# Performance work log

Hardware: AMD Instinct MI355X
Metric: run time of the kernel (lower is better)

Reference implementation:

```python
import jax, jax.numpy as jnp
import numpy as np

N, E = 25000, 400000
D, H, L = 64, 4, 3
DH = D  # per-head out dim (concat=False averages heads)
NODE_IN, EDGE_IN = 16, 4


def setup_inputs() -> dict:
    key = jax.random.key(0)
    ks = jax.random.split(key, 24)
    s = 0.05
    inp = {
        "node_feat_in": jax.random.normal(ks[0], (N, NODE_IN), jnp.float32),
        "edge_index_in": jax.random.randint(ks[1], (2, E), 0, N, jnp.int32),
        "edge_attr_in": jax.random.normal(ks[2], (E, EDGE_IN), jnp.float32),
        # initial embeddings
        "W_node": jax.random.normal(ks[3], (NODE_IN, D), jnp.float32) * s,
        "b_node": jnp.zeros((D,), jnp.float32),
        "W_edge": jax.random.normal(ks[4], (EDGE_IN, D), jnp.float32) * s,
        "b_edge": jnp.zeros((D,), jnp.float32),
        # GATv2Conv params, stacked over layers
        "Wl": jax.random.normal(ks[5], (L, D, H * DH), jnp.float32) * s,
        "bl": jnp.zeros((L, H * DH), jnp.float32),
        "Wr": jax.random.normal(ks[6], (L, D, H * DH), jnp.float32) * s,
        "br": jnp.zeros((L, H * DH), jnp.float32),
        "We": jax.random.normal(ks[7], (L, D, H * DH), jnp.float32) * s,
        "att": jax.random.normal(ks[8], (L, H, DH), jnp.float32) * s,
        "conv_b": jnp.zeros((L, D), jnp.float32),
        # LayerNorm
        "ln_g": jnp.ones((L, D), jnp.float32),
        "ln_b": jnp.zeros((L, D), jnp.float32),
        # edge update MLP: Linear(3D->D), ReLU, Linear(D->D)
        "euW1": jax.random.normal(ks[9], (L, 3 * D, D), jnp.float32) * s,
        "eub1": jnp.zeros((L, D), jnp.float32),
        "euW2": jax.random.normal(ks[10], (L, D, D), jnp.float32) * s,
        "eub2": jnp.zeros((L, D), jnp.float32),
    }
    return inp


def _layernorm(x, g, b, eps=1e-5):
    mu = x.mean(-1, keepdims=True)
    var = ((x - mu) ** 2).mean(-1, keepdims=True)
    return (x - mu) * jax.lax.rsqrt(var + eps) * g + b


def _gatv2_conv(x, e, row, col, Wl, bl, Wr, br, We, att, cb):
    # PyG GATv2Conv(concat=False, edge_dim=D), eval mode (no dropout),
    # add_self_loops=True with fill_value='mean' on edge_attr.
    n = x.shape[0]
    xl = (x @ Wl + bl).reshape(n, H, DH)  # source transform
    xr = (x @ Wr + br).reshape(n, H, DH)  # target transform
    # self-loop edge attr = per-target mean of incoming edge attrs
    cnt = jax.ops.segment_sum(jnp.ones((e.shape[0],), x.dtype), col, num_segments=n)
    e_loop = jax.ops.segment_sum(e, col, num_segments=n) / jnp.maximum(cnt, 1.0)[:, None]
    ee = (jnp.concatenate([e, e_loop], 0) @ We).reshape(-1, H, DH)
    loop = jnp.arange(n, dtype=row.dtype)
    rowf = jnp.concatenate([row, loop])
    colf = jnp.concatenate([col, loop])
    msg = xl[rowf] + xr[colf] + ee                      # [E+N, H, DH]
    score = jnp.sum(jax.nn.leaky_relu(msg, 0.2) * att, -1)  # [E+N, H]
    # segment softmax over incoming edges of each target node
    m = jax.ops.segment_max(score, colf, num_segments=n)
    a = jnp.exp(score - m[colf])
    a = a / jax.ops.segment_sum(a, colf, num_segments=n)[colf]
    out = jax.ops.segment_sum(a[..., None] * xl[rowf], colf, num_segments=n)  # [N,H,DH]
    return out.mean(1) + cb  # concat=False -> head mean, plus bias


def reference(node_feat_in, edge_index_in, edge_attr_in, W_node, b_node, W_edge,
              b_edge, Wl, bl, Wr, br, We, att, conv_b, ln_g, ln_b, euW1, eub1,
              euW2, eub2):
    row, col = edge_index_in[0], edge_index_in[1]
    x = jax.nn.relu(node_feat_in @ W_node + b_node)
    e = jax.nn.relu(edge_attr_in @ W_edge + b_edge)
    for i in range(L):
        upd = _gatv2_conv(x, e, row, col, Wl[i], bl[i], Wr[i], br[i], We[i],
                          att[i], conv_b[i])
        x = jax.nn.relu(_layernorm(x + upd, ln_g[i], ln_b[i]))
        eu_in = jnp.concatenate([x[row], x[col], e], -1)  # [E, 3D]
        e_upd = jax.nn.relu(eu_in @ euW1[i] + eub1[i]) @ euW2[i] + eub2[i]
        e = jax.nn.relu(e + e_upd)
    return x, e
```

## Files before the change

### kernel.cpp

```cpp
#include <hip/hip_runtime.h>
#include <hip/hip_bf16.h>
#include <cstdint>
#include <cstddef>

constexpr int kN  = 25000;
constexpr int kE  = 400000;
constexpr int kEN = kE + kN;
constexpr int kD  = 64;
constexpr int kH  = 4;
constexpr int kHD = 256;

typedef __attribute__((ext_vector_type(8))) short short8;
typedef __attribute__((ext_vector_type(4))) float f32x4;

__device__ __forceinline__ float lrelu02(float x){ return x > 0.f ? x : 0.2f*x; }
__device__ __forceinline__ unsigned short f2bf(float f){
  __hip_bfloat16 h = __float2bfloat16(f);
  return *reinterpret_cast<unsigned short*>(&h);
}
__device__ __forceinline__ float bf2f(unsigned short u){
  return __uint_as_float(((unsigned)u) << 16);
}
__device__ __forceinline__ float bf_lo(unsigned u){ return __uint_as_float(u << 16); }
__device__ __forceinline__ float bf_hi(unsigned u){ return __uint_as_float(u & 0xffff0000u); }
__device__ __forceinline__ unsigned pack_bf2(float a, float b){
  return ((unsigned)f2bf(a)) | (((unsigned)f2bf(b)) << 16);
}

__global__ void k_deg(const int* __restrict__ col, int* __restrict__ deg){
  int i = blockIdx.x*256 + threadIdx.x;
  if (i < kE) atomicAdd(&deg[col[i]], 1);
}

__global__ void k_scan(const int* __restrict__ deg, int* __restrict__ col_start){
  __shared__ int lds[1024];
  __shared__ int carry_s;
  int t = threadIdx.x;
  if (t == 0) carry_s = 0;
  __syncthreads();
  for (int base = 0; base < kN; base += 1024){
    int v = (base + t < kN) ? deg[base + t] : 0;
    lds[t] = v; __syncthreads();
    for (int off = 1; off < 1024; off <<= 1){
      int add = (t >= off) ? lds[t - off] : 0;
      __syncthreads();
      lds[t] += add;
      __syncthreads();
    }
    int incl = lds[t];
    int carry = carry_s;
    if (base + t < kN) col_start[base + t] = carry + incl - v;
    __syncthreads();
    if (t == 0) carry_s = carry + lds[1023];
    __syncthreads();
  }
  if (t == 0) col_start[kN] = carry_s;
}

__global__ void k_fill(const int* __restrict__ col, const int* __restrict__ col_start,
                       int* __restrict__ fill, int* __restrict__ edge_ids){
  int i = blockIdx.x*256 + threadIdx.x;
  if (i < kE){
    int c = col[i];
    int p = atomicAdd(&fill[c], 1);
    edge_ids[col_start[c] + p] = i;
  }
}

__global__ void k_permrc(const int* __restrict__ edge_ids, const int* __restrict__ row,
                         const int* __restrict__ col, int* __restrict__ rowp,
                         int2* __restrict__ rc2){
  int p = blockIdx.x*256 + threadIdx.x;
  if (p < kE){
    int eid = edge_ids[p];
    int r = row[eid], c = col[eid];
    rowp[p] = r;
    rc2[p] = make_int2(r, c);
  }
}

__global__ void k_prep(const float* __restrict__ We, unsigned short* __restrict__ WeT){
  int idx = blockIdx.x*256 + threadIdx.x;
  if (idx >= 3*256*64) return;
  int l = idx >> 14, j = (idx >> 6) & 255, k = idx & 63;
  WeT[idx] = f2bf(We[(size_t)l*16384 + k*256 + j]);
}

__global__ void k_prep2(const float* __restrict__ euW1, const float* __restrict__ euW2,
                        unsigned short* __restrict__ W1cT, unsigned short* __restrict__ W2T){
  int idx = blockIdx.x*256 + threadIdx.x;
  if (idx >= 3*64*64) return;
  int l = idx >> 12, rem = idx & 4095, d = rem >> 6, k = rem & 63;
  W1cT[idx] = f2bf(euW1[(size_t)l*192*64 + (size_t)(128+k)*64 + d]);
  W2T[idx]  = f2bf(euW2[(size_t)l*64*64  + (size_t)k*64 + d]);
}

__global__ void k_x0(const float* __restrict__ nf, const float* __restrict__ W,
                     const float* __restrict__ b, float* __restrict__ x){
  int i = blockIdx.x*256 + threadIdx.x;
  if (i >= kN*kD) return;
  int n = i >> 6, d = i & 63;
  float acc = b[d];
#pragma unroll
  for (int k = 0; k < 16; k++) acc += nf[n*16 + k] * W[k*64 + d];
  x[i] = fmaxf(acc, 0.f);
}

__global__ void k_e0p(const int* __restrict__ edge_ids,
                      const float* __restrict__ ea, const float* __restrict__ W,
                      const float* __restrict__ b,
                      unsigned short* __restrict__ ebf_perm){
  long long i = (long long)blockIdx.x*256 + threadIdx.x;
  if (i >= (long long)kE*kD) return;
  int p = (int)(i >> 6), d = (int)(i & 63);
  int eid = edge_ids[p];
  float acc = b[d];
#pragma unroll
  for (int k = 0; k < 4; k++) acc += ea[eid*4 + k] * W[k*64 + d];
  ebf_perm[i] = f2bf(fmaxf(acc, 0.f));
}

#define XLR_NPB 8
__global__ __launch_bounds__(256) void k_xlr(const float* __restrict__ x,
    const float* __restrict__ Wl, const float* __restrict__ bl,
    const float* __restrict__ Wr, const float* __restrict__ br,
    unsigned short* __restrict__ xl_bf, unsigned short* __restrict__ xr_bf){
  __shared__ float xs[XLR_NPB*64];
  int j = threadIdx.x;
  int n0 = blockIdx.x * XLR_NPB;
  for (int i = j; i < XLR_NPB*64; i += 256){
    int n = n0 + (i >> 6);
    xs[i] = (n < kN) ? x[(size_t)n*64 + (i & 63)] : 0.f;
  }
  __syncthreads();
  float accl[XLR_NPB], accr[XLR_NPB];
  float blv = bl[j], brv = br[j];
#pragma unroll
  for (int t = 0; t < XLR_NPB; t++){ accl[t] = blv; accr[t] = brv; }
  for (int k = 0; k < 64; k++){
    float wl = Wl[k*kHD + j], wr = Wr[k*kHD + j];
#pragma unroll
    for (int t = 0; t < XLR_NPB; t++){
      float xv = xs[t*64 + k];
      accl[t] += xv * wl; accr[t] += xv * wr;
    }
  }
#pragma unroll
  for (int t = 0; t < XLR_NPB; t++){
    int n = n0 + t;
    if (n < kN){
      xl_bf[(size_t)n*kHD + j] = f2bf(accl[t]);
      xr_bf[(size_t)n*kHD + j] = f2bf(accr[t]);
    }
  }
}

__global__ __launch_bounds__(256) void k_eloop(const unsigned short* __restrict__ ebf_perm,
    const int* __restrict__ col_start, unsigned short* __restrict__ eloop_bf){
  int wave = threadIdx.x >> 6, lane = threadIdx.x & 63;
  int n = blockIdx.x*4 + wave;
  if (n >= kN) return;
  int s0 = col_start[n], s1 = col_start[n+1];
  float acc = 0.f;
  for (int p = s0; p < s1; p++)
    acc += bf2f(ebf_perm[(size_t)p*64 + lane]);
  int dg = s1 - s0;
  eloop_bf[(size_t)n*64 + lane] = f2bf(acc / (float)(dg > 0 ? dg : 1));
}

#define SC_G 2048
#define SC_MAXT 13
__global__ __launch_bounds__(256) void k_score_mfma(
    const unsigned short* __restrict__ ebf_perm,
    const unsigned short* __restrict__ eloop_bf,
    const unsigned short* __restrict__ xl_bf,
    const unsigned short* __restrict__ xr_bf,
    const int2* __restrict__ rc2,
    const unsigned short* __restrict__ WeT,
    const float* __restrict__ att,
    float* __restrict__ score)
{
  int lane = threadIdx.x & 63;
  int h    = threadIdx.x >> 6;
  int e16  = lane & 15;
  int kb   = lane >> 4;

  short8 A[4][2];
  uint2 attp[4];
#pragma unroll
  for (int mt = 0; mt < 4; mt++){
    const unsigned short* arow = WeT + (size_t)(h*64 + mt*16 + e16)*64 + kb*8;
    A[mt][0] = *(const short8*)(arow);
    A[mt][1] = *(const short8*)(arow + 32);
    f32x4 av = *(const f32x4*)(att + h*64 + mt*16 + kb*4);
    attp[mt].x = pack_bf2(av[0], av[1]);
    attp[mt].y = pack_bf2(av[2], av[3]);
  }

  constexpr int NT = (kEN + 15)/16;
  int t0 = blockIdx.x;

  int2 rcs[SC_MAXT];
#pragma unroll
  for (int t = 0; t < SC_MAXT; t++){
    int tile = t0 + t*SC_G;
    if (tile < NT){
      int p = tile*16 + e16;
      int pc = (p < kEN) ? p : 0;
      if (pc < kE) rcs[t] = rc2[pc];
      else         rcs[t] = make_int2(pc - kE, pc - kE);
    } else {
      rcs[t] = make_int2(0, 0);
    }
  }

#pragma unroll
  for (int t = 0; t < SC_MAXT; t++){
    int tile = t0 + t*SC_G;
    if (tile >= NT) break;
    int p = tile*16 + e16;
    int pc = (p < kEN) ? p : 0;
    bool isE = pc < kE;
    const unsigned short* erow = isE ? (ebf_perm + (size_t)pc*64)
                                     : (eloop_bf + (size_t)(pc - kE)*64);
    short8 b0 = *(const short8*)(erow + kb*8);
    short8 b1 = *(const short8*)(erow + 32 + kb*8);
    const unsigned short* xl_ = xl_bf + (size_t)rcs[t].x*kHD + h*64;
    const unsigned short* xr_ = xr_bf + (size_t)rcs[t].y*kHD + h*64;
    uint2 xlu[4], xru[4];
#pragma unroll
    for (int mt = 0; mt < 4; mt++){
      xlu[mt] = *(const uint2*)(xl_ + mt*16 + kb*4);
      xru[mt] = *(const uint2*)(xr_ + mt*16 + kb*4);
    }
    float sc = 0.f;
#pragma unroll
    for (int mt = 0; mt < 4; mt++){
      f32x4 acc = {0.f,0.f,0.f,0.f};
      acc = __builtin_amdgcn_mfma_f32_16x16x32_bf16(A[mt][0], b0, acc, 0, 0, 0);
      acc = __builtin_amdgcn_mfma_f32_16x16x32_bf16(A[mt][1], b1, acc, 0, 0, 0);
      sc += lrelu02(acc[0] + bf_lo(xlu[mt].x) + bf_lo(xru[mt].x)) * bf_lo(attp[mt].x);
      sc += lrelu02(acc[1] + bf_hi(xlu[mt].x) + bf_hi(xru[mt].x)) * bf_hi(attp[mt].x);
      sc += lrelu02(acc[2] + bf_lo(xlu[mt].y) + bf_lo(xru[mt].y)) * bf_lo(attp[mt].y);
      sc += lrelu02(acc[3] + bf_hi(xlu[mt].y) + bf_hi(xru[mt].y)) * bf_hi(attp[mt].y);
    }
    sc += __shfl_xor(sc, 16);
    sc += __shfl_xor(sc, 32);
    int wp = tile*16 + lane;
    if (lane < 16 && wp < kEN) score[(size_t)wp*kH + h] = sc;
  }
}

__global__ __launch_bounds__(256) void k_agg_ln(
    const unsigned short* __restrict__ xl_bf, const float* __restrict__ score,
    const int* __restrict__ rowp, const int* __restrict__ col_start,
    const float* __restrict__ conv_b, const float* __restrict__ ln_g,
    const float* __restrict__ ln_b, float* __restrict__ x){
  int wv = threadIdx.x >> 6, l = threadIdx.x & 63;
  int n = blockIdx.x*4 + wv;
  if (n >= kN) return;
  int h = l >> 4;
  int s0 = col_start[n], s1 = col_start[n+1];

  float sc_self = score[(size_t)(kE + n)*kH + h];
  float m = sc_self;
  for (int p = s0; p < s1; p++)
    m = fmaxf(m, score[(size_t)p*kH + h]);

  float w0 = __expf(sc_self - m);
  float s = w0;
  float a0, a1, a2, a3;
  {
    uint2 u = *(const uint2*)(xl_bf + (size_t)n*kHD + l*4);
    a0 = w0*bf_lo(u.x); a1 = w0*bf_hi(u.x);
    a2 = w0*bf_lo(u.y); a3 = w0*bf_hi(u.y);
  }
  int p = s0;
  for (; p + 4 <= s1; p += 4){
    float e0 = __expf(score[(size_t)(p+0)*kH + h] - m);
    float e1 = __expf(score[(size_t)(p+1)*kH + h] - m);
    float e2 = __expf(score[(size_t)(p+2)*kH + h] - m);
    float e3 = __expf(score[(size_t)(p+3)*kH + h] - m);
    int r0 = rowp[p], r1 = rowp[p+1], r2 = rowp[p+2], r3 = rowp[p+3];
    uint2 u0 = *(const uint2*)(xl_bf + (size_t)r0*kHD + l*4);
    uint2 u1 = *(const uint2*)(xl_bf + (size_t)r1*kHD + l*4);
    uint2 u2 = *(const uint2*)(xl_bf + (size_t)r2*kHD + l*4);
    uint2 u3 = *(const uint2*)(xl_bf + (size_t)r3*kHD + l*4);
    s += e0 + e1 + e2 + e3;
    a0 += e0*bf_lo(u0.x) + e1*bf_lo(u1.x) + e2*bf_lo(u2.x) + e3*bf_lo(u3.x);
    a1 += e0*bf_hi(u0.x) + e1*bf_hi(u1.x) + e2*bf_hi(u2.x) + e3*bf_hi(u3.x);
    a2 += e0*bf_lo(u0.y) + e1*bf_lo(u1.y) + e2*bf_lo(u2.y) + e3*bf_lo(u3.y);
    a3 += e0*bf_hi(u0.y) + e1*bf_hi(u1.y) + e2*bf_hi(u2.y) + e3*bf_hi(u3.y);
  }
  for (; p < s1; p++){
    float ew = __expf(score[(size_t)p*kH + h] - m);
    int r = rowp[p];
    uint2 u = *(const uint2*)(xl_bf + (size_t)r*kHD + l*4);
    s += ew;
    a0 += ew*bf_lo(u.x); a1 += ew*bf_hi(u.x);
    a2 += ew*bf_lo(u.y); a3 += ew*bf_hi(u.y);
  }
  float inv = 1.f / s;
  a0 *= inv; a1 *= inv; a2 *= inv; a3 *= inv;
  a0 += __shfl_xor(a0, 16); a0 += __shfl_xor(a0, 32);
  a1 += __shfl_xor(a1, 16); a1 += __shfl_xor(a1, 32);
  a2 += __shfl_xor(a2, 16); a2 += __shfl_xor(a2, 32);
  a3 += __shfl_xor(a3, 16); a3 += __shfl_xor(a3, 32);
  int d0 = (l & 15)*4;
  f32x4 cb = *(const f32x4*)(conv_b + d0);
  f32x4 xv = *(const f32x4*)(x + (size_t)n*64 + d0);
  float y0 = xv[0] + a0*0.25f + cb[0];
  float y1 = xv[1] + a1*0.25f + cb[1];
  float y2 = xv[2] + a2*0.25f + cb[2];
  float y3 = xv[3] + a3*0.25f + cb[3];
  float part = y0 + y1 + y2 + y3;
  part += __shfl_xor(part, 1); part += __shfl_xor(part, 2);
  part += __shfl_xor(part, 4); part += __shfl_xor(part, 8);
  float mu = part * (1.f/64.f);
  float f0 = y0 - mu, f1 = y1 - mu, f2 = y2 - mu, f3 = y3 - mu;
  float vp = f0*f0 + f1*f1 + f2*f2 + f3*f3;
  vp += __shfl_xor(vp, 1); vp += __shfl_xor(vp, 2);
  vp += __shfl_xor(vp, 4); vp += __shfl_xor(vp, 8);
  float rstd = rsqrtf(vp * (1.f/64.f) + 1e-5f);
  f32x4 gv = *(const f32x4*)(ln_g + d0);
  f32x4 bv = *(const f32x4*)(ln_b + d0);
  if (l < 16){
    f32x4 o;
    o[0] = fmaxf(f0*rstd*gv[0] + bv[0], 0.f);
    o[1] = fmaxf(f1*rstd*gv[1] + bv[1], 0.f);
    o[2] = fmaxf(f2*rstd*gv[2] + bv[2], 0.f);
    o[3] = fmaxf(f3*rstd*gv[3] + bv[3], 0.f);
    *(f32x4*)(x + (size_t)n*64 + d0) = o;
  }
}

#define PQ_NPB 16
__global__ __launch_bounds__(256) void k_pq(const float* __restrict__ x,
    const float* __restrict__ W1, const float* __restrict__ b1,
    unsigned short* __restrict__ P_bf, unsigned short* __restrict__ Q_bf){
  __shared__ float xs[PQ_NPB*64];
  int tid = threadIdx.x;
  int j = tid & 63;
  int s = tid >> 6;
  int n0 = blockIdx.x * PQ_NPB;
  for (int i = tid; i < PQ_NPB*64; i += 256){
    int n = n0 + (i >> 6);
    xs[i] = (n < kN) ? x[(size_t)n*64 + (i & 63)] : 0.f;
  }
  __syncthreads();
  float accP[4], accQ[4];
  float b1v = b1[j];
#pragma unroll
  for (int t = 0; t < 4; t++){ accP[t] = b1v; accQ[t] = 0.f; }
  for (int k = 0; k < 64; k++){
    float wa = W1[k*64 + j];
    float wb = W1[(64 + k)*64 + j];
#pragma unroll
    for (int t = 0; t < 4; t++){
      float xv = xs[(s*4 + t)*64 + k];
      accP[t] += xv * wa; accQ[t] += xv * wb;
    }
  }
#pragma unroll
  for (int t = 0; t < 4; t++){
    int n = n0 + s*4 + t;
    if (n < kN){
      P_bf[(size_t)n*64 + j] = f2bf(accP[t]);
      Q_bf[(size_t)n*64 + j] = f2bf(accQ[t]);
    }
  }
}

__global__ __launch_bounds__(256) void k_mlp_mfma(
    unsigned short* __restrict__ ebf_perm,
    float* __restrict__ eout_scatter,
    const int* __restrict__ edge_ids,
    const unsigned short* __restrict__ P_bf, const unsigned short* __restrict__ Q_bf,
    const unsigned short* __restrict__ W1cT,
    const unsigned short* __restrict__ W2T,
    const float* __restrict__ b2,
    const int2* __restrict__ rc2)
{
  __shared__ unsigned short Hl[4][1024];
  int lane = threadIdx.x & 63, wv = threadIdx.x >> 6;
  int e16 = lane & 15, g = lane >> 4;
  int swz = (e16 & 7) << 4;
  char* Hw = (char*)Hl[wv];
  bool last = (eout_scatter != nullptr);

  short8 a1[4][2], a2[4][2];
#pragma unroll
  for (int mt = 0; mt < 4; mt++){
#pragma unroll
    for (int c = 0; c < 2; c++){
      a1[mt][c] = *(const short8*)(W1cT + (size_t)(mt*16 + e16)*64 + c*32 + g*8);
      a2[mt][c] = *(const short8*)(W2T  + (size_t)(mt*16 + e16)*64 + c*32 + g*8);
    }
  }
  f32x4 b2v[4];
#pragma unroll
  for (int mt = 0; mt < 4; mt++) b2v[mt] = *(const f32x4*)(b2 + mt*16 + g*4);

  int wid = (blockIdx.x*256 + threadIdx.x) >> 6;
  int nw  = (gridDim.x*256) >> 6;
  for (int tile = wid; tile < kE/16; tile += nw){
    int p = tile*16 + e16;
    int2 rc = rc2[p];
    const unsigned short* erow = ebf_perm + (size_t)p*64;
    short8 eb0 = *(const short8*)(erow + g*8);
    short8 eb1 = *(const short8*)(erow + 32 + g*8);
    const unsigned short* Pr = P_bf + (size_t)rc.x*64;
    const unsigned short* Qc = Q_bf + (size_t)rc.y*64;

#pragma unroll
    for (int mt = 0; mt < 4; mt++){
      f32x4 acc = {0.f,0.f,0.f,0.f};
      acc = __builtin_amdgcn_mfma_f32_16x16x32_bf16(a1[mt][0], eb0, acc, 0, 0, 0);
      acc = __builtin_amdgcn_mfma_f32_16x16x32_bf16(a1[mt][1], eb1, acc, 0, 0, 0);
      uint2 pu = *(const uint2*)(Pr + mt*16 + g*4);
      uint2 qu = *(const uint2*)(Qc + mt*16 + g*4);
      float h0 = fmaxf(acc[0] + bf_lo(pu.x) + bf_lo(qu.x), 0.f);
      float h1 = fmaxf(acc[1] + bf_hi(pu.x) + bf_hi(qu.x), 0.f);
      float h2 = fmaxf(acc[2] + bf_lo(pu.y) + bf_lo(qu.y), 0.f);
      float h3 = fmaxf(acc[3] + bf_hi(pu.y) + bf_hi(qu.y), 0.f);
      uint2 pk; pk.x = pack_bf2(h0, h1); pk.y = pack_bf2(h2, h3);
      *(uint2*)(Hw + (((e16 << 7) + (mt << 5) + (g << 3)) ^ swz)) = pk;
    }
    short8 hb0 = *(const short8*)(Hw + (((e16 << 7)      + (g << 4)) ^ swz));
    short8 hb1 = *(const short8*)(Hw + (((e16 << 7) + 64 + (g << 4)) ^ swz));

    int oe = last ? edge_ids[p] : 0;
#pragma unroll
    for (int mt = 0; mt < 4; mt++){
      f32x4 o = {0.f,0.f,0.f,0.f};
      o = __builtin_amdgcn_mfma_f32_16x16x32_bf16(a2[mt][0], hb0, o, 0, 0, 0);
      o = __builtin_amdgcn_mfma_f32_16x16x32_bf16(a2[mt][1], hb1, o, 0, 0, 0);
      size_t off = (size_t)p*64 + mt*16 + g*4;
      uint2 u = *(const uint2*)(ebf_perm + off);
      f32x4 eo;
      eo[0] = bf_lo(u.x); eo[1] = bf_hi(u.x); eo[2] = bf_lo(u.y); eo[3] = bf_hi(u.y);
      f32x4 ne;
      ne[0] = fmaxf(eo[0] + o[0] + b2v[mt][0], 0.f);
      ne[1] = fmaxf(eo[1] + o[1] + b2v[mt][1], 0.f);
      ne[2] = fmaxf(eo[2] + o[2] + b2v[mt][2], 0.f);
      ne[3] = fmaxf(eo[3] + o[3] + b2v[mt][3], 0.f);
      if (!last){
        uint2 po; po.x = pack_bf2(ne[0], ne[1]); po.y = pack_bf2(ne[2], ne[3]);
        *(uint2*)(ebf_perm + off) = po;
      } else {
        *(f32x4*)(eout_scatter + (size_t)oe*64 + mt*16 + g*4) = ne;
      }
    }
  }
}

extern "C" void kernel_launch(void* const* d_in, const int* in_sizes, int n_in,
                              void* d_out, int out_size, void* d_ws, size_t ws_size,
                              hipStream_t stream) {
  const float* node_feat = (const float*)d_in[0];
  const int*   edge_idx  = (const int*)d_in[1];
  const float* edge_attr = (const float*)d_in[2];
  const float* W_node = (const float*)d_in[3];
  const float* b_node = (const float*)d_in[4];
  const float* W_edge = (const float*)d_in[5];
  const float* b_edge = (const float*)d_in[6];
  const float* Wl   = (const float*)d_in[7];
  const float* bl   = (const float*)d_in[8];
  const float* Wr   = (const float*)d_in[9];
  const float* br   = (const float*)d_in[10];
  const float* We   = (const float*)d_in[11];
  const float* att  = (const float*)d_in[12];
  const float* cvb  = (const float*)d_in[13];
  const float* lng  = (const float*)d_in[14];
  const float* lnb  = (const float*)d_in[15];
  const float* euW1 = (const float*)d_in[16];
  const float* eub1 = (const float*)d_in[17];
  const float* euW2 = (const float*)d_in[18];
  const float* eub2 = (const float*)d_in[19];

  const int* row = edge_idx;
  const int* col = edge_idx + kE;

  float* x = (float*)d_out;
  float* e_out = (float*)d_out + (size_t)kN*kD;

  char* p = (char*)d_ws;
  auto carve = [&](size_t bytes)->void*{
    void* r = (void*)p;
    p += (bytes + 255) & ~(size_t)255;
    return r;
  };
  unsigned short* xl_bf    = (unsigned short*)carve((size_t)kN*kHD*2);
  unsigned short* xr_bf    = (unsigned short*)carve((size_t)kN*kHD*2);
  unsigned short* P_bf     = (unsigned short*)carve((size_t)kN*kD*2);
  unsigned short* Q_bf     = (unsigned short*)carve((size_t)kN*kD*2);
  unsigned short* ebf_perm = (unsigned short*)carve((size_t)kE*kD*2);
  unsigned short* eloop_bf = (unsigned short*)carve((size_t)kN*kD*2);
  unsigned short* WeT      = (unsigned short*)carve((size_t)3*kHD*kD*2);
  unsigned short* W1cT     = (unsigned short*)carve((size_t)3*kD*kD*2);
  unsigned short* W2T      = (unsigned short*)carve((size_t)3*kD*kD*2);
  float* score  = (float*)carve((size_t)kEN*kH*4);
  int* deg      = (int*)carve((size_t)kN*4);
  int* col_start= (int*)carve((size_t)(kN+1)*4);
  int* fill     = (int*)carve((size_t)kN*4);
  int* edge_ids = (int*)carve((size_t)kE*4);
  int* rowp     = (int*)carve((size_t)kE*4);
  int2* rc2     = (int2*)carve((size_t)kE*8);

  hipMemsetAsync(deg, 0, (size_t)kN*4, stream);
  hipMemsetAsync(fill, 0, (size_t)kN*4, stream);
  k_deg<<<(kE+255)/256, 256, 0, stream>>>(col, deg);
  k_scan<<<1, 1024, 0, stream>>>(deg, col_start);
  k_fill<<<(kE+255)/256, 256, 0, stream>>>(col, col_start, fill, edge_ids);
  k_permrc<<<(kE+255)/256, 256, 0, stream>>>(edge_ids, row, col, rowp, rc2);

  k_prep<<<192, 256, 0, stream>>>(We, WeT);
  k_prep2<<<48, 256, 0, stream>>>(euW1, euW2, W1cT, W2T);
  k_x0<<<(kN*kD+255)/256, 256, 0, stream>>>(node_feat, W_node, b_node, x);
  k_e0p<<<(int)(((size_t)kE*kD+255)/256), 256, 0, stream>>>(edge_ids, edge_attr, W_edge,
                                                            b_edge, ebf_perm);

  for (int i = 0; i < 3; i++){
    const float* Wl_i  = Wl  + (size_t)i*kD*kHD;
    const float* bl_i  = bl  + (size_t)i*kHD;
    const float* Wr_i  = Wr  + (size_t)i*kD*kHD;
    const float* br_i  = br  + (size_t)i*kHD;
    const float* att_i = att + (size_t)i*kHD;
    const float* cvb_i = cvb + (size_t)i*kD;
    const float* lng_i = lng + (size_t)i*kD;
    const float* lnb_i = lnb + (size_t)i*kD;
    const float* W1_i  = euW1 + (size_t)i*192*64;
    const float* b1_i  = eub1 + (size_t)i*kD;
    const float* b2_i  = eub2 + (size_t)i*kD;
    const unsigned short* WeT_i  = WeT  + (size_t)i*kHD*kD;
    const unsigned short* W1cT_i = W1cT + (size_t)i*kD*kD;
    const unsigned short* W2T_i  = W2T  + (size_t)i*kD*kD;

    k_xlr<<<(kN + XLR_NPB - 1)/XLR_NPB, 256, 0, stream>>>(x, Wl_i, bl_i, Wr_i, br_i,
                                                          xl_bf, xr_bf);
    k_eloop<<<(kN + 3)/4, 256, 0, stream>>>(ebf_perm, col_start, eloop_bf);
    k_score_mfma<<<SC_G, 256, 0, stream>>>(ebf_perm, eloop_bf, xl_bf, xr_bf,
                                           rc2, WeT_i, att_i, score);
    k_agg_ln<<<(kN + 3)/4, 256, 0, stream>>>(xl_bf, score, rowp, col_start,
                                             cvb_i, lng_i, lnb_i, x);
    k_pq<<<(kN + PQ_NPB - 1)/PQ_NPB, 256, 0, stream>>>(x, W1_i, b1_i, P_bf, Q_bf);
    k_mlp_mfma<<<2048, 256, 0, stream>>>(ebf_perm, (i < 2) ? nullptr : e_out,
                                         edge_ids, P_bf, Q_bf, W1cT_i, W2T_i, b2_i,
                                         rc2);
  }
}
```

Measured before the change: 981.5 us.

## Compute segment max via atomics in score kernel; prefetch MLP edge indices

```diff
diff --git a/kernel.cpp b/kernel.cpp
--- a/kernel.cpp
+++ b/kernel.cpp
@@ -25,6 +25,14 @@
 __device__ __forceinline__ float bf_hi(unsigned u){ return __uint_as_float(u & 0xffff0000u); }
 __device__ __forceinline__ unsigned pack_bf2(float a, float b){
   return ((unsigned)f2bf(a)) | (((unsigned)f2bf(b)) << 16);
+}
+__device__ __forceinline__ unsigned encf(float f){
+  unsigned u = __float_as_uint(f);
+  return (u & 0x80000000u) ? ~u : (u | 0x80000000u);
+}
+__device__ __forceinline__ float decf(unsigned e){
+  return (e & 0x80000000u) ? __uint_as_float(e & 0x7fffffffu)
+                           : __uint_as_float(~e);
 }
 
 __global__ void k_deg(const int* __restrict__ col, int* __restrict__ deg){
@@ -178,7 +186,8 @@
     const int2* __restrict__ rc2,
     const unsigned short* __restrict__ WeT,
     const float* __restrict__ att,
-    float* __restrict__ score)
+    float* __restrict__ score,
+    unsigned* __restrict__ smax)
 {
   int lane = threadIdx.x & 63;
   int h    = threadIdx.x >> 6;
@@ -247,12 +256,17 @@
     sc += __shfl_xor(sc, 16);
     sc += __shfl_xor(sc, 32);
     int wp = tile*16 + lane;
-    if (lane < 16 && wp < kEN) score[(size_t)wp*kH + h] = sc;
+    if (lane < 16 && wp < kEN){
+      score[(size_t)wp*kH + h] = sc;
+      int n = (wp < kE) ? rcs[t].y : (wp - kE);
+      atomicMax(&smax[n*kH + h], encf(sc));
+    }
   }
 }
 
 __global__ __launch_bounds__(256) void k_agg_ln(
     const unsigned short* __restrict__ xl_bf, const float* __restrict__ score,
+    const unsigned* __restrict__ smax,
     const int* __restrict__ rowp, const int* __restrict__ col_start,
     const float* __restrict__ conv_b, const float* __restrict__ ln_g,
     const float* __restrict__ ln_b, float* __restrict__ x){
@@ -262,10 +276,8 @@
   int h = l >> 4;
   int s0 = col_start[n], s1 = col_start[n+1];
 
+  float m = decf(smax[n*kH + h]);
   float sc_self = score[(size_t)(kE + n)*kH + h];
-  float m = sc_self;
-  for (int p = s0; p < s1; p++)
-    m = fmaxf(m, score[(size_t)p*kH + h]);
 
   float w0 = __expf(sc_self - m);
   float s = w0;
@@ -371,6 +383,8 @@
   }
 }
 
+#define MLP_G 2048
+#define MLP_MAXT 4
 __global__ __launch_bounds__(256) void k_mlp_mfma(
     unsigned short* __restrict__ ebf_perm,
     float* __restrict__ eout_scatter,
@@ -401,16 +415,27 @@
 #pragma unroll
   for (int mt = 0; mt < 4; mt++) b2v[mt] = *(const f32x4*)(b2 + mt*16 + g*4);
 
+  constexpr int MT = kE/16;
+  constexpr int NW = MLP_G*4;
   int wid = (blockIdx.x*256 + threadIdx.x) >> 6;
-  int nw  = (gridDim.x*256) >> 6;
-  for (int tile = wid; tile < kE/16; tile += nw){
+
+  int2 rcs[MLP_MAXT];
+#pragma unroll
+  for (int t = 0; t < MLP_MAXT; t++){
+    int tile = wid + t*NW;
+    rcs[t] = (tile < MT) ? rc2[tile*16 + e16] : make_int2(0, 0);
+  }
+
+#pragma unroll
+  for (int t = 0; t < MLP_MAXT; t++){
+    int tile = wid + t*NW;
+    if (tile >= MT) break;
     int p = tile*16 + e16;
-    int2 rc = rc2[p];
     const unsigned short* erow = ebf_perm + (size_t)p*64;
     short8 eb0 = *(const short8*)(erow + g*8);
     short8 eb1 = *(const short8*)(erow + 32 + g*8);
-    const unsigned short* Pr = P_bf + (size_t)rc.x*64;
-    const unsigned short* Qc = Q_bf + (size_t)rc.y*64;
+    const unsigned short* Pr = P_bf + (size_t)rcs[t].x*64;
+    const unsigned short* Qc = Q_bf + (size_t)rcs[t].y*64;
 
 #pragma unroll
     for (int mt = 0; mt < 4; mt++){
@@ -500,6 +525,7 @@
   unsigned short* W1cT     = (unsigned short*)carve((size_t)3*kD*kD*2);
   unsigned short* W2T      = (unsigned short*)carve((size_t)3*kD*kD*2);
   float* score  = (float*)carve((size_t)kEN*kH*4);
+  unsigned* smax= (unsigned*)carve((size_t)kN*kH*4);
   int* deg      = (int*)carve((size_t)kN*4);
   int* col_start= (int*)carve((size_t)(kN+1)*4);
   int* fill     = (int*)carve((size_t)kN*4);
@@ -539,13 +565,14 @@
     k_xlr<<<(kN + XLR_NPB - 1)/XLR_NPB, 256, 0, stream>>>(x, Wl_i, bl_i, Wr_i, br_i,
                                                           xl_bf, xr_bf);
     k_eloop<<<(kN + 3)/4, 256, 0, stream>>>(ebf_perm, col_start, eloop_bf);
+    hipMemsetAsync(smax, 0, (size_t)kN*kH*4, stream);
     k_score_mfma<<<SC_G, 256, 0, stream>>>(ebf_perm, eloop_bf, xl_bf, xr_bf,
-                                           rc2, WeT_i, att_i, score);
-    k_agg_ln<<<(kN + 3)/4, 256, 0, stream>>>(xl_bf, score, rowp, col_start,
+                                           rc2, WeT_i, att_i, score, smax);
+    k_agg_ln<<<(kN + 3)/4, 256, 0, stream>>>(xl_bf, score, smax, rowp, col_start,
                                              cvb_i, lng_i, lnb_i, x);
     k_pq<<<(kN + PQ_NPB - 1)/PQ_NPB, 256, 0, stream>>>(x, W1_i, b1_i, P_bf, Q_bf);
-    k_mlp_mfma<<<2048, 256, 0, stream>>>(ebf_perm, (i < 2) ? nullptr : e_out,
-                                         edge_ids, P_bf, Q_bf, W1cT_i, W2T_i, b2_i,
-                                         rc2);
-  }
-}
+    k_mlp_mfma<<<MLP_G, 256, 0, stream>>>(ebf_perm, (i < 2) ? nullptr : e_out,
+                                          edge_ids, P_bf, Q_bf, W1cT_i, W2T_i, b2_i,
+                                          rc2);
+  }
+}
```

After: 1.375 ms. +40.1%, slower.
